# Performance work log

Measured on AMD Instinct MI355X. Metric: run time of the kernel, lower is better.

Reference implementation:

```python
import jax, jax.numpy as jnp
import numpy as np

NUM_C = 1024
EMB = 512
HID = 512
BATCH = 64
SEQ = 512


def setup_inputs() -> dict:
    key = jax.random.key(0)
    ks = jax.random.split(key, 10)
    q = jax.random.randint(ks[0], (BATCH, SEQ), 0, NUM_C, dtype=jnp.int32)
    r = jax.random.randint(ks[1], (BATCH, SEQ), 0, 2, dtype=jnp.int32)
    s = 1.0 / np.sqrt(HID)
    emb = jax.random.normal(ks[2], (NUM_C * 2, EMB), dtype=jnp.float32)
    Wh_w = jax.random.uniform(ks[3], (HID, HID), jnp.float32, -s, s)
    Wh_b = jax.random.uniform(ks[4], (HID,), jnp.float32, -s, s)
    Wx_w = jax.random.uniform(ks[5], (HID, EMB), jnp.float32, -s, s)
    Wx_b = jax.random.uniform(ks[6], (HID,), jnp.float32, -s, s)
    tau = jnp.ones((HID,), jnp.float32)
    Wo_w = jax.random.uniform(ks[7], (NUM_C, HID), jnp.float32, -s, s)
    Wo_b = jax.random.uniform(ks[8], (NUM_C,), jnp.float32, -s, s)
    return {"q": q, "r": r, "emb": emb, "Wh_w": Wh_w, "Wh_b": Wh_b,
            "Wx_w": Wx_w, "Wx_b": Wx_b, "tau": tau, "Wo_w": Wo_w, "Wo_b": Wo_b}


def reference(q, r, emb, Wh_w, Wh_b, Wx_w, Wx_b, tau, Wo_w, Wo_b):
    # interaction embedding: x = q + num_c * r
    idx = q + NUM_C * r                      # [B, S]
    xemb = emb[idx]                          # [B, S, E]
    # precompute input projection for all timesteps (faithful: same sum)
    xproj = jnp.einsum('bse,he->bsh', xemb, Wx_w) + Wx_b + Wh_b  # [B, S, H]

    def step(h, xp_t):
        # liquid time-constant cell update
        dh = (-h + jnp.tanh(h @ Wh_w.T + xp_t)) / tau
        h_new = h + dh
        return h_new, h_new

    h0 = jnp.zeros((q.shape[0], HID), xemb.dtype)
    _, hs = jax.lax.scan(step, h0, jnp.swapaxes(xproj, 0, 1))  # hs: [S, B, H]
    outputs = jnp.swapaxes(hs, 0, 1)         # [B, S, H]
    # dropout is identity at inference
    y = jax.nn.sigmoid(jnp.einsum('bsh,ch->bsc', outputs, Wo_w) + Wo_b)
    return y
```

## Files before the change

kernel.cpp:

```cpp
#include <hip/hip_runtime.h>
#include <hip/hip_bf16.h>

#define NUM_C 1024
#define EMB   512
#define HID   512
#define BATCH 64
#define SEQ   512

typedef short bf16x8 __attribute__((ext_vector_type(8)));
typedef float f32x4  __attribute__((ext_vector_type(4)));

__device__ __forceinline__ unsigned short f2bf(float x) {
    unsigned u = __float_as_uint(x);
    u += 0x7fffu + ((u >> 16) & 1u);
    return (unsigned short)(u >> 16);
}
__device__ __forceinline__ float uaf(unsigned u) { return __uint_as_float(u); }

__device__ __forceinline__ float ftanh(float x) {
    float e = __expf(2.f * x);
    return 1.f - 2.f / (e + 1.f);
}

__global__ __launch_bounds__(256) void f32_to_bf16(const float* __restrict__ src,
                                                   unsigned short* __restrict__ dst, int n) {
    int i = blockIdx.x * 256 + threadIdx.x;
    if (i < n) dst[i] = f2bf(src[i]);
}

__global__ __launch_bounds__(256)
void gemm_nt_f32(const float* __restrict__ A, const float* __restrict__ B,
                 float* __restrict__ C, int M, int N, int K,
                 const float* __restrict__ bias1, const float* __restrict__ bias2) {
    __shared__ float As[64][33];
    __shared__ float Bs[64][33];

    const int n0 = blockIdx.x * 64;
    const int m0 = blockIdx.y * 64;
    const int tid = threadIdx.x;
    const int tx = tid & 15;
    const int ty = tid >> 4;

    float acc[4][4] = {{0.f}};

    for (int k0 = 0; k0 < K; k0 += 32) {
        #pragma unroll
        for (int i = 0; i < 2; ++i) {
            int f   = tid * 2 + i;
            int row = f >> 3;
            int kf  = f & 7;
            float4 va = *(const float4*)&A[(size_t)(m0 + row) * K + k0 + kf * 4];
            float4 vb = *(const float4*)&B[(size_t)(n0 + row) * K + k0 + kf * 4];
            As[row][kf * 4 + 0] = va.x; As[row][kf * 4 + 1] = va.y;
            As[row][kf * 4 + 2] = va.z; As[row][kf * 4 + 3] = va.w;
            Bs[row][kf * 4 + 0] = vb.x; Bs[row][kf * 4 + 1] = vb.y;
            Bs[row][kf * 4 + 2] = vb.z; Bs[row][kf * 4 + 3] = vb.w;
        }
        __syncthreads();
        #pragma unroll
        for (int kk = 0; kk < 32; ++kk) {
            float a[4], b[4];
            #pragma unroll
            for (int i = 0; i < 4; ++i) a[i] = As[ty * 4 + i][kk];
            #pragma unroll
            for (int j = 0; j < 4; ++j) b[j] = Bs[tx * 4 + j][kk];
            #pragma unroll
            for (int i = 0; i < 4; ++i)
                #pragma unroll
                for (int j = 0; j < 4; ++j)
                    acc[i][j] += a[i] * b[j];
        }
        __syncthreads();
    }

    float bb[4];
    #pragma unroll
    for (int j = 0; j < 4; ++j) {
        int n = n0 + tx * 4 + j;
        bb[j] = bias1[n] + bias2[n];
    }
    #pragma unroll
    for (int i = 0; i < 4; ++i) {
        size_t m = (size_t)(m0 + ty * 4 + i);
        float4 ov;
        ov.x = acc[i][0] + bb[0]; ov.y = acc[i][1] + bb[1];
        ov.z = acc[i][2] + bb[2]; ov.w = acc[i][3] + bb[3];
        *(float4*)&C[m * N + n0 + tx * 4] = ov;
    }
}

#define PREFETCH(E_PF, ID, STEP)                                               \
    if (fin && (STEP) < SEQ)                                                   \
        E_PF = emb_proj[(size_t)ID[STEP] * HID + sl * 64 + lane];

#define FINISHX(PS, E, H, HSW, ST, PW)                                         \
    {                                                                          \
        float pre = E;                                                         \
        _Pragma("unroll")                                                      \
        for (int m = 0; m < 8; ++m) pre += PS[m * 64 + lane];                  \
        float hn = H + (ftanh(pre) - H) * rtau;                                \
        H = hn;                                                                \
        unsigned us = f2bf(hn);                                                \
        unsigned ot = (unsigned)__shfl_xor((int)us, 1);                        \
        unsigned word = us | (ot << 16);                                       \
        if (!(lane & 1))                                                       \
            __hip_atomic_store(&HSW[(ST) * 256 + sl * 32 + (lane >> 1)],       \
                               word, __ATOMIC_RELAXED,                         \
                               __HIP_MEMORY_SCOPE_AGENT);                      \
        PW = (unsigned)__shfl((int)word, (2 * lane) & 63);                     \
    }

#define POLLX(HSW, ST, PW)                                                     \
    {                                                                          \
        unsigned word = 0;                                                     \
        if (lane < 32) {                                                       \
            unsigned* ap = &HSW[(ST) * 256 + w * 32 + lane];                   \
            word = __hip_atomic_load(ap, __ATOMIC_RELAXED,                     \
                                     __HIP_MEMORY_SCOPE_AGENT);                \
            while ((word & 0xffffu) == 0x7f7fu) {                              \
                __builtin_amdgcn_s_sleep(1);                                   \
                word = __hip_atomic_load(ap, __ATOMIC_RELAXED,                 \
                                         __HIP_MEMORY_SCOPE_AGENT);            \
            }                                                                  \
        }                                                                      \
        PW = word;                                                             \
    }

#define MACX(PW, PS)                                                           \
    {                                                                          \
        float a0 = 0.f, a1 = 0.f, a2 = 0.f, a3 = 0.f;                          \
        _Pragma("unroll")                                                      \
        for (int t = 0; t < 32; t += 2) {                                      \
            unsigned w0 = (unsigned)__builtin_amdgcn_readlane((int)PW, t);     \
            unsigned w1 = (unsigned)__builtin_amdgcn_readlane((int)PW, t + 1); \
            a0 = fmaf(wf[2 * t],     uaf(w0 << 16),         a0);               \
            a1 = fmaf(wf[2 * t + 1], uaf(w0 & 0xffff0000u), a1);               \
            a2 = fmaf(wf[2 * t + 2], uaf(w1 << 16),         a2);               \
            a3 = fmaf(wf[2 * t + 3], uaf(w1 & 0xffff0000u), a3);               \
        }                                                                      \
        PS[w * 64 + lane] = (a0 + a1) + (a2 + a3);                             \
    }

__global__ __launch_bounds__(512, 2)
void ltc_scan8(const int* __restrict__ q, const int* __restrict__ r,
               const float* __restrict__ emb_proj, const float* __restrict__ Wh,
               const float* __restrict__ tau, unsigned short* __restrict__ hs_bf) {
    __shared__ float psA[512], psB[512];
    __shared__ int   idA[512], idB[512];

    const int tid  = threadIdx.x;
    const int sl   = blockIdx.x >> 5;
    const int bp   = blockIdx.x & 31;
    const int bA   = bp * 2, bB = bA + 1;
    const int lane = tid & 63;
    const int w    = tid >> 6;

    float wf[64];
    {
        const float* wrow = Wh + (size_t)(sl * 64 + lane) * 512 + w * 64;
        #pragma unroll
        for (int i = 0; i < 16; ++i) {
            float4 v = ((const float4*)wrow)[i];
            wf[4 * i + 0] = v.x; wf[4 * i + 1] = v.y;
            wf[4 * i + 2] = v.z; wf[4 * i + 3] = v.w;
        }
    }

    idA[tid] = q[bA * SEQ + tid] + NUM_C * r[bA * SEQ + tid];
    idB[tid] = q[bB * SEQ + tid] + NUM_C * r[bB * SEQ + tid];

    const bool fin = (w == sl);
    float rtau = 0.f, hA = 0.f, hB = 0.f, eA = 0.f, eB = 0.f;
    unsigned pwA = 0, pwB = 0;
    if (fin) rtau = 1.0f / tau[sl * 64 + lane];

    unsigned* hswA = (unsigned*)(hs_bf + (size_t)bA * SEQ * HID);
    unsigned* hswB = (unsigned*)(hs_bf + (size_t)bB * SEQ * HID);
    __syncthreads();

    if (fin) eA = emb_proj[(size_t)idA[0] * HID + sl * 64 + lane];

    for (int s = 0; s < SEQ; ++s) {
        float pfB = 0.f;
        PREFETCH(pfB, idB, s);
        if (fin) {
            if (s > 0) FINISHX(psB, eB, hB, hswB, s - 1, pwB);
            eB = pfB;
        } else if (s > 0) {
            POLLX(hswA, s - 1, pwA);
        }
        MACX(pwA, psA);
        __syncthreads();

        float pfA = 0.f;
        PREFETCH(pfA, idA, s + 1);
        if (fin) {
            FINISHX(psA, eA, hA, hswA, s, pwA);
            eA = pfA;
        } else if (s > 0) {
            POLLX(hswB, s - 1, pwB);
        }
        MACX(pwB, psB);
        __syncthreads();
    }

    if (fin) FINISHX(psB, eB, hB, hswB, SEQ - 1, pwB);
}

__global__ __launch_bounds__(256)
void gemm_out_bf16(const unsigned short* __restrict__ A,
                   const unsigned short* __restrict__ B,
                   const float* __restrict__ bias,
                   float* __restrict__ C, int M) {
    __shared__ __align__(16) unsigned short As[128 * 32];
    __shared__ __align__(16) unsigned short Bs[128 * 32];

    const int tid = threadIdx.x;
    const int n0 = blockIdx.x * 128;
    const int m0 = blockIdx.y * 128;
    const int w  = tid >> 6;
    const int l  = tid & 63;
    const int wr = w >> 1, wc = w & 1;
    const int lr = l & 15;
    const int lq = l >> 4;

    f32x4 acc[4][4];
    #pragma unroll
    for (int i = 0; i < 4; ++i)
        #pragma unroll
        for (int jn = 0; jn < 4; ++jn)
            acc[i][jn] = (f32x4){0.f, 0.f, 0.f, 0.f};

    for (int k0 = 0; k0 < 512; k0 += 32) {
        #pragma unroll
        for (int p = 0; p < 2; ++p) {
            int flat = p * 256 + tid;
            int row  = flat >> 2;
            int c4   = flat & 3;
            *(uint4*)&As[row * 32 + c4 * 8] =
                *(const uint4*)&A[(size_t)(m0 + row) * 512 + k0 + c4 * 8];
            *(uint4*)&Bs[row * 32 + c4 * 8] =
                *(const uint4*)&B[(size_t)(n0 + row) * 512 + k0 + c4 * 8];
        }
        __syncthreads();

        bf16x8 af[4], bf[4];
        #pragma unroll
        for (int mf = 0; mf < 4; ++mf)
            af[mf] = *(const bf16x8*)&As[(wr * 64 + mf * 16 + lr) * 32 + lq * 8];
        #pragma unroll
        for (int nf = 0; nf < 4; ++nf)
            bf[nf] = *(const bf16x8*)&Bs[(wc * 64 + nf * 16 + lr) * 32 + lq * 8];

        #pragma unroll
        for (int mf = 0; mf < 4; ++mf)
            #pragma unroll
            for (int nf = 0; nf < 4; ++nf)
                acc[mf][nf] = __builtin_amdgcn_mfma_f32_16x16x32_bf16(
                    af[mf], bf[nf], acc[mf][nf], 0, 0, 0);
        __syncthreads();
    }

    #pragma unroll
    for (int mf = 0; mf < 4; ++mf) {
        #pragma unroll
        for (int nf = 0; nf < 4; ++nf) {
            int col = n0 + wc * 64 + nf * 16 + lr;
            float bb = bias[col];
            #pragma unroll
            for (int reg = 0; reg < 4; ++reg) {
                int rowm = m0 + wr * 64 + mf * 16 + lq * 4 + reg;
                float v = acc[mf][nf][reg] + bb;
                C[(size_t)rowm * 1024 + col] = 1.0f / (1.0f + expf(-v));
            }
        }
    }
}

extern "C" void kernel_launch(void* const* d_in, const int* in_sizes, int n_in,
                              void* d_out, int out_size, void* d_ws, size_t ws_size,
                              hipStream_t stream) {
    const int*   q    = (const int*)d_in[0];
    const int*   r    = (const int*)d_in[1];
    const float* emb  = (const float*)d_in[2];
    const float* Wh_w = (const float*)d_in[3];
    const float* Wh_b = (const float*)d_in[4];
    const float* Wx_w = (const float*)d_in[5];
    const float* Wx_b = (const float*)d_in[6];
    const float* tau  = (const float*)d_in[7];
    const float* Wo_w = (const float*)d_in[8];
    const float* Wo_b = (const float*)d_in[9];
    float* out = (float*)d_out;

    char* ws = (char*)d_ws;
    float*          emb_proj = (float*)ws;
    unsigned short* Wobf     = (unsigned short*)(ws + (4u << 20));
    unsigned short* hs_bf    = (unsigned short*)(ws + (5u << 20));

    hipMemsetAsync(hs_bf, 0x7F, (size_t)BATCH * SEQ * HID * 2, stream);

    f32_to_bf16<<<(1024 * 512) / 256, 256, 0, stream>>>(Wo_w, Wobf, 1024 * 512);

    gemm_nt_f32<<<dim3(512 / 64, 2048 / 64), 256, 0, stream>>>(
        emb, Wx_w, emb_proj, 2048, 512, 512, Wx_b, Wh_b);

    ltc_scan8<<<256, 512, 0, stream>>>(q, r, emb_proj, Wh_w, tau, hs_bf);

    gemm_out_bf16<<<dim3(1024 / 128, (BATCH * SEQ) / 128), 256, 0, stream>>>(
        hs_bf, Wobf, Wo_b, out, BATCH * SEQ);
}
```

Before: 873.9 us.

## Split scan to one batch per block and exchange fp32 hidden state

```diff
diff --git a/kernel.cpp b/kernel.cpp
--- a/kernel.cpp
+++ b/kernel.cpp
@@ -14,6 +14,9 @@
     unsigned u = __float_as_uint(x);
     u += 0x7fffu + ((u >> 16) & 1u);
     return (unsigned short)(u >> 16);
+}
+__device__ __forceinline__ unsigned pack2bf(float a, float b) {
+    return (unsigned)f2bf(a) | ((unsigned)f2bf(b) << 16);
 }
 __device__ __forceinline__ float uaf(unsigned u) { return __uint_as_float(u); }
 
@@ -89,69 +92,54 @@
     }
 }
 
-#define PREFETCH(E_PF, ID, STEP)                                               \
-    if (fin && (STEP) < SEQ)                                                   \
-        E_PF = emb_proj[(size_t)ID[STEP] * HID + sl * 64 + lane];
-
-#define FINISHX(PS, E, H, HSW, ST, PW)                                         \
-    {                                                                          \
-        float pre = E;                                                         \
+#define STEP9(PS_CUR, PS_NXT, S)                                               \
+    __syncthreads();                                                           \
+    if (fin) {                                                                 \
+        float pre = e;                                                         \
         _Pragma("unroll")                                                      \
-        for (int m = 0; m < 8; ++m) pre += PS[m * 64 + lane];                  \
-        float hn = H + (ftanh(pre) - H) * rtau;                                \
-        H = hn;                                                                \
-        unsigned us = f2bf(hn);                                                \
-        unsigned ot = (unsigned)__shfl_xor((int)us, 1);                        \
-        unsigned word = us | (ot << 16);                                       \
-        if (!(lane & 1))                                                       \
-            __hip_atomic_store(&HSW[(ST) * 256 + sl * 32 + (lane >> 1)],       \
-                               word, __ATOMIC_RELAXED,                         \
-                               __HIP_MEMORY_SCOPE_AGENT);                      \
-        PW = (unsigned)__shfl((int)word, (2 * lane) & 63);                     \
-    }
-
-#define POLLX(HSW, ST, PW)                                                     \
-    {                                                                          \
-        unsigned word = 0;                                                     \
-        if (lane < 32) {                                                       \
-            unsigned* ap = &HSW[(ST) * 256 + w * 32 + lane];                   \
-            word = __hip_atomic_load(ap, __ATOMIC_RELAXED,                     \
-                                     __HIP_MEMORY_SCOPE_AGENT);                \
-            while ((word & 0xffffu) == 0x7f7fu) {                              \
-                __builtin_amdgcn_s_sleep(1);                                   \
-                word = __hip_atomic_load(ap, __ATOMIC_RELAXED,                 \
-                                         __HIP_MEMORY_SCOPE_AGENT);            \
-            }                                                                  \
+        for (int m = 0; m < 8; ++m) pre += PS_CUR[m * 64 + lane];              \
+        float hn = h + (ftanh(pre) - h) * rtau;                                \
+        h = hn;                                                                \
+        __hip_atomic_store((unsigned*)&hxb[(S) * 512 + sl * 64 + lane],        \
+                           __float_as_uint(hn), __ATOMIC_RELAXED,              \
+                           __HIP_MEMORY_SCOPE_AGENT);                          \
+        if ((S) + 1 < SEQ)                                                     \
+            e = emb_proj[(size_t)ids[(S) + 1] * HID + sl * 64 + lane];         \
+    }                                                                          \
+    if ((S) + 1 < SEQ) {                                                       \
+        unsigned* ap = (unsigned*)&hxb[(S) * 512 + w * 64 + lane];             \
+        int wi = (int)__hip_atomic_load(ap, __ATOMIC_RELAXED,                  \
+                                        __HIP_MEMORY_SCOPE_AGENT);             \
+        while (((unsigned)wi & 0x7f800000u) == 0x7f800000u) {                  \
+            __builtin_amdgcn_s_sleep(1);                                       \
+            wi = (int)__hip_atomic_load(ap, __ATOMIC_RELAXED,                  \
+                                        __HIP_MEMORY_SCOPE_AGENT);             \
         }                                                                      \
-        PW = word;                                                             \
-    }
-
-#define MACX(PW, PS)                                                           \
-    {                                                                          \
         float a0 = 0.f, a1 = 0.f, a2 = 0.f, a3 = 0.f;                          \
         _Pragma("unroll")                                                      \
-        for (int t = 0; t < 32; t += 2) {                                      \
-            unsigned w0 = (unsigned)__builtin_amdgcn_readlane((int)PW, t);     \
-            unsigned w1 = (unsigned)__builtin_amdgcn_readlane((int)PW, t + 1); \
-            a0 = fmaf(wf[2 * t],     uaf(w0 << 16),         a0);               \
-            a1 = fmaf(wf[2 * t + 1], uaf(w0 & 0xffff0000u), a1);               \
-            a2 = fmaf(wf[2 * t + 2], uaf(w1 << 16),         a2);               \
-            a3 = fmaf(wf[2 * t + 3], uaf(w1 & 0xffff0000u), a3);               \
+        for (int t = 0; t < 64; t += 4) {                                      \
+            a0 = fmaf(wf[t + 0],                                               \
+                      uaf((unsigned)__builtin_amdgcn_readlane(wi, t + 0)), a0);\
+            a1 = fmaf(wf[t + 1],                                               \
+                      uaf((unsigned)__builtin_amdgcn_readlane(wi, t + 1)), a1);\
+            a2 = fmaf(wf[t + 2],                                               \
+                      uaf((unsigned)__builtin_amdgcn_readlane(wi, t + 2)), a2);\
+            a3 = fmaf(wf[t + 3],                                               \
+                      uaf((unsigned)__builtin_amdgcn_readlane(wi, t + 3)), a3);\
         }                                                                      \
-        PS[w * 64 + lane] = (a0 + a1) + (a2 + a3);                             \
-    }
-
-__global__ __launch_bounds__(512, 2)
-void ltc_scan8(const int* __restrict__ q, const int* __restrict__ r,
+        PS_NXT[w * 64 + lane] = (a0 + a1) + (a2 + a3);                         \
+    }
+
+__global__ __launch_bounds__(512, 4)
+void ltc_scan9(const int* __restrict__ q, const int* __restrict__ r,
                const float* __restrict__ emb_proj, const float* __restrict__ Wh,
-               const float* __restrict__ tau, unsigned short* __restrict__ hs_bf) {
+               const float* __restrict__ tau, float* __restrict__ hx) {
     __shared__ float psA[512], psB[512];
-    __shared__ int   idA[512], idB[512];
+    __shared__ int   ids[512];
 
     const int tid  = threadIdx.x;
-    const int sl   = blockIdx.x >> 5;
-    const int bp   = blockIdx.x & 31;
-    const int bA   = bp * 2, bB = bA + 1;
+    const int sl   = blockIdx.x >> 6;
+    const int b    = blockIdx.x & 63;
     const int lane = tid & 63;
     const int w    = tid >> 6;
 
@@ -166,49 +154,26 @@
         }
     }
 
-    idA[tid] = q[bA * SEQ + tid] + NUM_C * r[bA * SEQ + tid];
-    idB[tid] = q[bB * SEQ + tid] + NUM_C * r[bB * SEQ + tid];
-
-    const bool fin = (w == sl);
-    float rtau = 0.f, hA = 0.f, hB = 0.f, eA = 0.f, eB = 0.f;
-    unsigned pwA = 0, pwB = 0;
+    ids[tid] = q[b * SEQ + tid] + NUM_C * r[b * SEQ + tid];
+    psA[tid] = 0.f;
+
+    const bool fin = (w == 0);
+    float rtau = 0.f, h = 0.f, e = 0.f;
     if (fin) rtau = 1.0f / tau[sl * 64 + lane];
 
-    unsigned* hswA = (unsigned*)(hs_bf + (size_t)bA * SEQ * HID);
-    unsigned* hswB = (unsigned*)(hs_bf + (size_t)bB * SEQ * HID);
+    float* hxb = hx + (size_t)b * SEQ * HID;
     __syncthreads();
 
-    if (fin) eA = emb_proj[(size_t)idA[0] * HID + sl * 64 + lane];
-
-    for (int s = 0; s < SEQ; ++s) {
-        float pfB = 0.f;
-        PREFETCH(pfB, idB, s);
-        if (fin) {
-            if (s > 0) FINISHX(psB, eB, hB, hswB, s - 1, pwB);
-            eB = pfB;
-        } else if (s > 0) {
-            POLLX(hswA, s - 1, pwA);
-        }
-        MACX(pwA, psA);
-        __syncthreads();
-
-        float pfA = 0.f;
-        PREFETCH(pfA, idA, s + 1);
-        if (fin) {
-            FINISHX(psA, eA, hA, hswA, s, pwA);
-            eA = pfA;
-        } else if (s > 0) {
-            POLLX(hswB, s - 1, pwB);
-        }
-        MACX(pwB, psB);
-        __syncthreads();
-    }
-
-    if (fin) FINISHX(psB, eB, hB, hswB, SEQ - 1, pwB);
+    if (fin) e = emb_proj[(size_t)ids[0] * HID + sl * 64 + lane];
+
+    for (int s = 0; s < SEQ; s += 2) {
+        STEP9(psA, psB, s);
+        STEP9(psB, psA, s + 1);
+    }
 }
 
 __global__ __launch_bounds__(256)
-void gemm_out_bf16(const unsigned short* __restrict__ A,
+void gemm_out_bf16(const float* __restrict__ A,
                    const unsigned short* __restrict__ B,
                    const float* __restrict__ bias,
                    float* __restrict__ C, int M) {
@@ -237,8 +202,13 @@
             int flat = p * 256 + tid;
             int row  = flat >> 2;
             int c4   = flat & 3;
-            *(uint4*)&As[row * 32 + c4 * 8] =
-                *(const uint4*)&A[(size_t)(m0 + row) * 512 + k0 + c4 * 8];
+            const float* asrc = &A[(size_t)(m0 + row) * 512 + k0 + c4 * 8];
+            float4 v0 = ((const float4*)asrc)[0];
+            float4 v1 = ((const float4*)asrc)[1];
+            uint4 d;
+            d.x = pack2bf(v0.x, v0.y); d.y = pack2bf(v0.z, v0.w);
+            d.z = pack2bf(v1.x, v1.y); d.w = pack2bf(v1.z, v1.w);
+            *(uint4*)&As[row * 32 + c4 * 8] = d;
             *(uint4*)&Bs[row * 32 + c4 * 8] =
                 *(const uint4*)&B[(size_t)(n0 + row) * 512 + k0 + c4 * 8];
         }
@@ -295,17 +265,17 @@
     char* ws = (char*)d_ws;
     float*          emb_proj = (float*)ws;
     unsigned short* Wobf     = (unsigned short*)(ws + (4u << 20));
-    unsigned short* hs_bf    = (unsigned short*)(ws + (5u << 20));
-
-    hipMemsetAsync(hs_bf, 0x7F, (size_t)BATCH * SEQ * HID * 2, stream);
+    float*          hx       = (float*)(ws + (5u << 20));
+
+    hipMemsetAsync(hx, 0xFF, (size_t)BATCH * SEQ * HID * 4, stream);
 
     f32_to_bf16<<<(1024 * 512) / 256, 256, 0, stream>>>(Wo_w, Wobf, 1024 * 512);
 
     gemm_nt_f32<<<dim3(512 / 64, 2048 / 64), 256, 0, stream>>>(
         emb, Wx_w, emb_proj, 2048, 512, 512, Wx_b, Wh_b);
 
-    ltc_scan8<<<256, 512, 0, stream>>>(q, r, emb_proj, Wh_w, tau, hs_bf);
+    ltc_scan9<<<512, 512, 0, stream>>>(q, r, emb_proj, Wh_w, tau, hx);
 
     gemm_out_bf16<<<dim3(1024 / 128, (BATCH * SEQ) / 128), 256, 0, stream>>>(
-        hs_bf, Wobf, Wo_b, out, BATCH * SEQ);
-}
+        hx, Wobf, Wo_b, out, BATCH * SEQ);
+}
```

Measured after the change: 801.2 us. 1.09x faster.
